# Performance work log

Measured on AMD Instinct MI355X. Metric: run time of the kernel, lower is better.

Reference implementation:

```python
import jax, jax.numpy as jnp
import numpy as np
import math

B, S, D, H = 2, 2048, 1024, 16
DH = D // H  # dim_per_head = 64


def setup_inputs() -> dict:
    key = jax.random.key(0)
    ks = jax.random.split(key, 12)
    s = 1.0 / math.sqrt(D)
    return {
        "key": jax.random.normal(ks[0], (B, S, D), jnp.float32),
        "value": jax.random.normal(ks[1], (B, S, D), jnp.float32),
        "query": jax.random.normal(ks[2], (B, S, D), jnp.float32),
        "mask": jax.random.randint(ks[3], (B, S, S), 0, 2).astype(bool),
        "Wq": jax.random.normal(ks[4], (D, D), jnp.float32) * s,
        "bq": jnp.zeros((D,), jnp.float32),
        "Wk": jax.random.normal(ks[5], (D, D), jnp.float32) * s,
        "bk": jnp.zeros((D,), jnp.float32),
        "Wv": jax.random.normal(ks[6], (D, D), jnp.float32) * s,
        "bv": jnp.zeros((D,), jnp.float32),
        "Wo": jax.random.normal(ks[7], (D, D), jnp.float32) * s,
        "bo": jnp.zeros((D,), jnp.float32),
    }


def _shape(x):
    # [B, S, D] -> [B, H, S, DH]
    return x.reshape(B, -1, H, DH).transpose(0, 2, 1, 3)


def reference(key, value, query, mask, Wq, bq, Wk, bk, Wv, bv, Wo, bo):
    q = _shape(query @ Wq.T + bq)  # [B,H,Sq,DH]
    k = _shape(key @ Wk.T + bk)    # [B,H,Sk,DH]
    v = _shape(value @ Wv.T + bv)  # [B,H,Sk,DH]
    q = q / jnp.sqrt(jnp.asarray(DH, q.dtype))
    scores = jnp.einsum("bhqd,bhkd->bhqk", q, k)
    scores = jnp.where(mask[:, None, :, :], jnp.asarray(-1e18, scores.dtype), scores)
    attn = jax.nn.softmax(scores, axis=-1)
    # dropout is identity in eval/deterministic reference
    ctx = jnp.einsum("bhqk,bhkd->bhqd", attn, v)
    ctx = ctx.transpose(0, 2, 1, 3).reshape(B, -1, D)  # unshape
    return ctx @ Wo.T + bo
```

## Files before the change

kernel.cpp:

```cpp
#include <hip/hip_runtime.h>
#include <math.h>


constexpr int Bc  = 2;
constexpr int Sc  = 2048;
constexpr int Dc  = 1024;
constexpr int Hc  = 16;
constexpr int DHc = 64;
constexpr int BSc = Bc * Sc;

constexpr float LOG2E = 1.4426950408889634f;

typedef __bf16 bf16x8 __attribute__((ext_vector_type(8)));
typedef __bf16 bf16x4 __attribute__((ext_vector_type(4)));
typedef float  f32x4  __attribute__((ext_vector_type(4)));

#define GLDS16(gp, lp) __builtin_amdgcn_global_load_lds( \
    (const __attribute__((address_space(1))) void*)(gp), \
    (__attribute__((address_space(3))) void*)(lp), 16, 0, 0)

__global__ __launch_bounds__(256)
void wsplit(const float* __restrict__ W0, const float* __restrict__ W1,
            const float* __restrict__ W2, const float* __restrict__ W3,
            __bf16* __restrict__ out)
{
    const float* src[4] = {W0, W1, W2, W3};
    const int z = blockIdx.y;
    const size_t idx = ((size_t)blockIdx.x * 256 + threadIdx.x) * 4;
    const float4 v = *(const float4*)&src[z][idx];
    bf16x4 o;
    o[0] = (__bf16)v.x; o[1] = (__bf16)v.y; o[2] = (__bf16)v.z; o[3] = (__bf16)v.w;
    *(bf16x4*)&out[(size_t)z * Dc * Dc + idx] = o;
}

__device__ __forceinline__ void sweep128s(const float* __restrict__ A,
                                          const __bf16* __restrict__ Wh,
                                          __bf16* As, __bf16* Ws,
                                          int gm0, int gn0, f32x4 acc[4][4])
{
    const int tid  = threadIdx.x;
    const int w    = tid >> 6;
    const int lane = tid & 63;
    const int cc   = lane & 15;
    const int g    = lane >> 4;
    const int wm   = (w & 1) * 64;
    const int wn   = (w >> 1) * 64;

    for (int k0 = 0; k0 < Dc; k0 += 64) {
        __syncthreads();
#pragma unroll
        for (int r = 0; r < 4; ++r) {
            const int L  = r * 256 + tid;
            const int wr = L >> 3;
            const int sl = L & 7;
            const int c  = sl ^ (wr & 7);
            GLDS16(Wh + (size_t)(gn0 + wr) * Dc + k0 + c * 8,
                   (char*)Ws + (r * 256 + w * 64) * 16);
        }
#pragma unroll
        for (int i = 0; i < 8; ++i) {
            const int Lq = i * 256 + tid;
            const int ar = Lq >> 4;
            const int aq = Lq & 15;
            const float4 v = *(const float4*)&A[(size_t)(gm0 + ar) * Dc + k0 + aq * 4];
            const int off = ar * 128 +
                        ((((aq >> 1) ^ (ar & 7)) << 4) | ((aq & 1) << 3));
            bf16x4 hv;
            hv[0] = (__bf16)v.x; hv[1] = (__bf16)v.y;
            hv[2] = (__bf16)v.z; hv[3] = (__bf16)v.w;
            *(bf16x4*)((char*)As + off) = hv;
        }
        __syncthreads();
#pragma unroll
        for (int kk = 0; kk < 2; ++kk) {
            const int cb4 = (kk * 4 + g) << 4;
            bf16x8 af[4], bfr[4];
#pragma unroll
            for (int mt = 0; mt < 4; ++mt) {
                const int row = wm + mt * 16 + cc;
                af[mt] = *(const bf16x8*)((const char*)As + row * 128 +
                                          (cb4 ^ ((row & 7) << 4)));
            }
#pragma unroll
            for (int nt = 0; nt < 4; ++nt) {
                const int row = wn + nt * 16 + cc;
                bfr[nt] = *(const bf16x8*)((const char*)Ws + row * 128 +
                                           (cb4 ^ ((row & 7) << 4)));
            }
#pragma unroll
            for (int mt = 0; mt < 4; ++mt)
#pragma unroll
                for (int nt = 0; nt < 4; ++nt)
                    acc[mt][nt] = __builtin_amdgcn_mfma_f32_16x16x32_bf16(
                        af[mt], bfr[nt], acc[mt][nt], 0, 0, 0);
        }
    }
}

__device__ __forceinline__ void sweep64b(const __bf16* __restrict__ Ahi,
                                         const __bf16* __restrict__ Alo,
                                         const __bf16* __restrict__ Wh,
                                         __bf16* AsHi, __bf16* AsLo, __bf16* Ws,
                                         int gm0, int gn0, f32x4 acc[2][4])
{
    const int tid  = threadIdx.x;
    const int w    = tid >> 6;
    const int lane = tid & 63;
    const int cc   = lane & 15;
    const int g    = lane >> 4;
    const int wm   = (w & 1) * 32;
    const int wn   = (w >> 1) * 64;

    for (int k0 = 0; k0 < Dc; k0 += 64) {
        __syncthreads();
#pragma unroll
        for (int r = 0; r < 4; ++r) {
            const int L  = r * 256 + tid;
            const int wr = L >> 3;
            const int sl = L & 7;
            const int c  = sl ^ (wr & 7);
            GLDS16(Wh + (size_t)(gn0 + wr) * Dc + k0 + c * 8,
                   (char*)Ws + (r * 256 + w * 64) * 16);
        }
#pragma unroll
        for (int r = 0; r < 2; ++r) {
            const int L  = r * 256 + tid;
            const int wr = L >> 3;
            const int sl = L & 7;
            const int c  = sl ^ (wr & 7);
            GLDS16(Ahi + (size_t)(gm0 + wr) * Dc + k0 + c * 8,
                   (char*)AsHi + (r * 256 + w * 64) * 16);
            GLDS16(Alo + (size_t)(gm0 + wr) * Dc + k0 + c * 8,
                   (char*)AsLo + (r * 256 + w * 64) * 16);
        }
        __syncthreads();
#pragma unroll
        for (int kk = 0; kk < 2; ++kk) {
            const int cb4 = (kk * 4 + g) << 4;
            bf16x8 ahi[2], alo[2], bfr[4];
#pragma unroll
            for (int mt = 0; mt < 2; ++mt) {
                const int row = wm + mt * 16 + cc;
                const int off = row * 128 + (cb4 ^ ((row & 7) << 4));
                ahi[mt] = *(const bf16x8*)((const char*)AsHi + off);
                alo[mt] = *(const bf16x8*)((const char*)AsLo + off);
            }
#pragma unroll
            for (int nt = 0; nt < 4; ++nt) {
                const int row = wn + nt * 16 + cc;
                bfr[nt] = *(const bf16x8*)((const char*)Ws + row * 128 +
                                           (cb4 ^ ((row & 7) << 4)));
            }
#pragma unroll
            for (int mt = 0; mt < 2; ++mt)
#pragma unroll
                for (int nt = 0; nt < 4; ++nt) {
                    acc[mt][nt] = __builtin_amdgcn_mfma_f32_16x16x32_bf16(
                        ahi[mt], bfr[nt], acc[mt][nt], 0, 0, 0);
                    acc[mt][nt] = __builtin_amdgcn_mfma_f32_16x16x32_bf16(
                        alo[mt], bfr[nt], acc[mt][nt], 0, 0, 0);
                }
        }
    }
}

__global__ __launch_bounds__(256)
void qkv_mfma(const float* __restrict__ query, const float* __restrict__ key,
              const float* __restrict__ value, const __bf16* __restrict__ Whi,
              const float* __restrict__ bq, const float* __restrict__ bk,
              const float* __restrict__ bv,
              __bf16* __restrict__ Qo, __bf16* __restrict__ Ko, __bf16* __restrict__ Vt)
{
    __shared__ __align__(16) __bf16 As[8192];
    __shared__ __align__(16) __bf16 Ws[8192];

    const int z = blockIdx.z;
    const float* A    = (z == 0) ? query : (z == 1) ? key : value;
    const float* bias = (z == 0) ? bq    : (z == 1) ? bk  : bv;
    const float scale = (z == 0) ? 0.125f * LOG2E : 1.0f;
    const __bf16* Wh  = Whi + (size_t)z * Dc * Dc;

    const int gm0 = blockIdx.x * 128;
    const int gn0 = blockIdx.y * 128;

    f32x4 acc[4][4];
#pragma unroll
    for (int mt = 0; mt < 4; ++mt)
#pragma unroll
        for (int nt = 0; nt < 4; ++nt) acc[mt][nt] = {0.f, 0.f, 0.f, 0.f};

    sweep128s(A, Wh, As, Ws, gm0, gn0, acc);

    const int tid = threadIdx.x;
    const int w = tid >> 6, lane = tid & 63;
    const int cc = lane & 15, g = lane >> 4;
    const int wm = (w & 1) * 64, wn = (w >> 1) * 64;

    float bias4[4];
#pragma unroll
    for (int nt = 0; nt < 4; ++nt) bias4[nt] = bias[gn0 + wn + nt * 16 + cc];

    if (z == 2) {
#pragma unroll
        for (int mt = 0; mt < 4; ++mt)
#pragma unroll
            for (int nt = 0; nt < 4; ++nt) {
                const int col = gn0 + wn + nt * 16 + cc;
                const int h = col >> 6, dh = col & 63;
                const int row0 = gm0 + wm + mt * 16 + g * 4;
                const int b = row0 >> 11, s0 = row0 & 2047;
                bf16x4 vv;
#pragma unroll
                for (int reg = 0; reg < 4; ++reg)
                    vv[reg] = (__bf16)(acc[mt][nt][reg] + bias4[nt]);
                *(bf16x4*)&Vt[(((size_t)(b * Hc + h)) * DHc + dh) * Sc + s0] = vv;
            }
    } else {
        __bf16* O = (z == 0) ? Qo : Ko;
#pragma unroll
        for (int mt = 0; mt < 4; ++mt)
#pragma unroll
            for (int nt = 0; nt < 4; ++nt) {
                const int col = gn0 + wn + nt * 16 + cc;
                const int h = col >> 6, dh = col & 63;
#pragma unroll
                for (int reg = 0; reg < 4; ++reg) {
                    const int row = gm0 + wm + mt * 16 + g * 4 + reg;
                    const int b = row >> 11, s = row & 2047;
                    O[(((size_t)(b * Hc + h)) * Sc + s) * DHc + dh] =
                        (__bf16)((acc[mt][nt][reg] + bias4[nt]) * scale);
                }
            }
    }
}

__global__ __launch_bounds__(256)
void out_mfma(const __bf16* __restrict__ ctxHi, const __bf16* __restrict__ ctxLo,
              const __bf16* __restrict__ Wohi,
              const float* __restrict__ bo, float* __restrict__ out)
{
    __shared__ __align__(16) __bf16 AsHi[4096];
    __shared__ __align__(16) __bf16 AsLo[4096];
    __shared__ __align__(16) __bf16 Ws[8192];

    const int gm0 = blockIdx.x * 64;
    const int gn0 = blockIdx.y * 128;

    f32x4 acc[2][4];
#pragma unroll
    for (int mt = 0; mt < 2; ++mt)
#pragma unroll
        for (int nt = 0; nt < 4; ++nt) acc[mt][nt] = {0.f, 0.f, 0.f, 0.f};

    sweep64b(ctxHi, ctxLo, Wohi, AsHi, AsLo, Ws, gm0, gn0, acc);

    const int tid = threadIdx.x;
    const int w = tid >> 6, lane = tid & 63;
    const int cc = lane & 15, g = lane >> 4;
    const int wm = (w & 1) * 32, wn = (w >> 1) * 64;

    float bias4[4];
#pragma unroll
    for (int nt = 0; nt < 4; ++nt) bias4[nt] = bo[gn0 + wn + nt * 16 + cc];

#pragma unroll
    for (int mt = 0; mt < 2; ++mt)
#pragma unroll
        for (int nt = 0; nt < 4; ++nt) {
            const int col = gn0 + wn + nt * 16 + cc;
#pragma unroll
            for (int reg = 0; reg < 4; ++reg) {
                const int row = gm0 + wm + mt * 16 + g * 4 + reg;
                out[(size_t)row * Dc + col] = acc[mt][nt][reg] + bias4[nt];
            }
        }
}

__global__ __launch_bounds__(256)
void mask_pack(const int* __restrict__ mask, unsigned long long* __restrict__ out)
{
    const int lane = threadIdx.x & 63;
    const size_t waveBase = ((size_t)blockIdx.x * 4 + (threadIdx.x >> 6)) * 256;
    unsigned long long b0 = __ballot(mask[waveBase + lane]        != 0);
    unsigned long long b1 = __ballot(mask[waveBase + 64 + lane]   != 0);
    unsigned long long b2 = __ballot(mask[waveBase + 128 + lane]  != 0);
    unsigned long long b3 = __ballot(mask[waveBase + 192 + lane]  != 0);
    if (lane == 0) {
        unsigned long long* dst = out + (waveBase >> 6);
        dst[0] = b0; dst[1] = b1; dst[2] = b2; dst[3] = b3;
    }
}

__global__ __launch_bounds__(256, 2)
void attn_mfma(const __bf16* __restrict__ Q, const __bf16* __restrict__ K,
               const __bf16* __restrict__ Vt,
               const unsigned long long* __restrict__ mp,
               __bf16* __restrict__ ctxHi, __bf16* __restrict__ ctxLo)
{
    __shared__ __align__(16) char smem[40960];

    const int tid  = threadIdx.x;
    const int w    = tid >> 6;
    const int lane = tid & 63;
    const int cc   = lane & 15;
    const int g    = lane >> 4;
    const int bh   = blockIdx.y;
    const int b    = bh >> 4;
    const int h    = bh & 15;
    const int qw   = blockIdx.x * 128 + w * 32;

    const __bf16* Qb  = Q  + (size_t)bh * Sc * DHc;
    const __bf16* Kb  = K  + (size_t)bh * Sc * DHc;
    const __bf16* Vtb = Vt + (size_t)bh * DHc * Sc;

    char* Pw = smem + 32768 + w * 2048;

    bf16x8 qa[2][2];
#pragma unroll
    for (int mt = 0; mt < 2; ++mt) {
        qa[mt][0] = *(const bf16x8*)&Qb[(size_t)(qw + mt * 16 + cc) * DHc + g * 8];
        qa[mt][1] = *(const bf16x8*)&Qb[(size_t)(qw + mt * 16 + cc) * DHc + 32 + g * 8];
    }

    f32x4 o[2][4] = {};
    float l[2][4] = {};

    const int ci[2] = {tid, 256 + tid};
    int  rowi[2], ski[2];
#pragma unroll
    for (int i = 0; i < 2; ++i) {
        rowi[i] = ci[i] >> 3;
        const int sl = ci[i] & 7;
        ski[i] = sl ^ (rowi[i] & 7);
    }

#pragma unroll
    for (int i = 0; i < 2; ++i) {
        GLDS16(Kb + (size_t)rowi[i] * DHc + ski[i] * 8,
               smem + ci[i] * 16);
        GLDS16(Vtb + (size_t)rowi[i] * Sc + ski[i] * 8,
               smem + 8192 + ci[i] * 16);
    }

    for (int it = 0; it < 32; ++it) {
        const int k0 = it * 64;
        char* Ks = smem + (it & 1) * 16384;
        char* Vs = Ks + 8192;

        __syncthreads();

        if (it + 1 < 32) {
            char* Kn = smem + ((it + 1) & 1) * 16384;
            const int kn = k0 + 64;
#pragma unroll
            for (int i = 0; i < 2; ++i) {
                GLDS16(Kb + (size_t)(kn + rowi[i]) * DHc + ski[i] * 8,
                       Kn + ci[i] * 16);
                GLDS16(Vtb + (size_t)rowi[i] * Sc + kn + ski[i] * 8,
                       Kn + 8192 + ci[i] * 16);
            }
        }

        unsigned long long mw[2][4];
#pragma unroll
        for (int mt = 0; mt < 2; ++mt)
#pragma unroll
            for (int r = 0; r < 4; ++r)
                mw[mt][r] = mp[(size_t)(b * Sc + qw + mt * 16 + g * 4 + r) * (Sc / 64)
                               + (k0 >> 6)];

        f32x4 sc[2][4];
#pragma unroll
        for (int nt = 0; nt < 4; ++nt) {
            const int row = nt * 16 + cc;
            const int rx  = (row & 7) << 4;
            const bf16x8 kb0 = *(const bf16x8*)(Ks + row * 128 + ((g << 4) ^ rx));
            const bf16x8 kb1 = *(const bf16x8*)(Ks + row * 128 + ((64 + (g << 4)) ^ rx));
            f32x4 z0 = {-24.f, -24.f, -24.f, -24.f};
            z0 = __builtin_amdgcn_mfma_f32_16x16x32_bf16(qa[0][0], kb0, z0, 0, 0, 0);
            z0 = __builtin_amdgcn_mfma_f32_16x16x32_bf16(qa[0][1], kb1, z0, 0, 0, 0);
            sc[0][nt] = z0;
            f32x4 z1 = {-24.f, -24.f, -24.f, -24.f};
            z1 = __builtin_amdgcn_mfma_f32_16x16x32_bf16(qa[1][0], kb0, z1, 0, 0, 0);
            z1 = __builtin_amdgcn_mfma_f32_16x16x32_bf16(qa[1][1], kb1, z1, 0, 0, 0);
            sc[1][nt] = z1;
        }

        bf16x8 pa[2][2];
#pragma unroll
        for (int mt = 0; mt < 2; ++mt) {
            unsigned mlo[4], mhi[4];
#pragma unroll
            for (int r = 0; r < 4; ++r) {
                const unsigned long long sh = mw[mt][r] >> cc;
                mlo[r] = (unsigned)sh;
                mhi[r] = (unsigned)(sh >> 32);
            }
#pragma unroll
            for (int nt = 0; nt < 4; ++nt)
#pragma unroll
                for (int r = 0; r < 4; ++r) {
                    float p = __builtin_amdgcn_exp2f(sc[mt][nt][r]);
                    const unsigned bit =
                        (nt == 0) ? (mlo[r] & 1u) :
                        (nt == 1) ? (mlo[r] & 0x10000u) :
                        (nt == 2) ? (mhi[r] & 1u) : (mhi[r] & 0x10000u);
                    p = bit ? 0.f : p;
                    l[mt][r] += p;
                    *(__bf16*)(Pw + (g * 4 + r) * 128 +
                               (((nt ^ g) << 5) | (cc << 1))) = (__bf16)p;
                }
            const int sw = (cc >> 2) << 5;
            pa[mt][0] = *(const bf16x8*)(Pw + cc * 128 + ((g * 16) ^ sw));
            pa[mt][1] = *(const bf16x8*)(Pw + cc * 128 + ((64 + g * 16) ^ sw));
        }

#pragma unroll
        for (int nt = 0; nt < 4; ++nt) {
            const int row = nt * 16 + cc;
            const int rx  = (row & 7) << 4;
            const bf16x8 vb0 = *(const bf16x8*)(Vs + row * 128 + ((g << 4) ^ rx));
            const bf16x8 vb1 = *(const bf16x8*)(Vs + row * 128 + ((64 + (g << 4)) ^ rx));
            o[0][nt] = __builtin_amdgcn_mfma_f32_16x16x32_bf16(pa[0][0], vb0, o[0][nt], 0, 0, 0);
            o[0][nt] = __builtin_amdgcn_mfma_f32_16x16x32_bf16(pa[0][1], vb1, o[0][nt], 0, 0, 0);
            o[1][nt] = __builtin_amdgcn_mfma_f32_16x16x32_bf16(pa[1][0], vb0, o[1][nt], 0, 0, 0);
            o[1][nt] = __builtin_amdgcn_mfma_f32_16x16x32_bf16(pa[1][1], vb1, o[1][nt], 0, 0, 0);
        }
    }

#pragma unroll
    for (int off = 1; off < 16; off <<= 1)
#pragma unroll
        for (int mt = 0; mt < 2; ++mt)
#pragma unroll
            for (int r = 0; r < 4; ++r)
                l[mt][r] += __shfl_xor(l[mt][r], off, 16);

#pragma unroll
    for (int mt = 0; mt < 2; ++mt)
#pragma unroll
        for (int r = 0; r < 4; ++r) {
            const float inv = 1.0f / l[mt][r];
            const int q = qw + mt * 16 + g * 4 + r;
#pragma unroll
            for (int nt = 0; nt < 4; ++nt) {
                const size_t idx = ((size_t)b * Sc + q) * Dc + h * 64 + nt * 16 + cc;
                const float v = o[mt][nt][r] * inv;
                const __bf16 hi = (__bf16)v;
                ctxHi[idx] = hi;
                ctxLo[idx] = (__bf16)(v - (float)hi);
            }
        }
}

extern "C" void kernel_launch(void* const* d_in, const int* in_sizes, int n_in,
                              void* d_out, int out_size, void* d_ws, size_t ws_size,
                              hipStream_t stream)
{
    const float* key   = (const float*)d_in[0];
    const float* value = (const float*)d_in[1];
    const float* query = (const float*)d_in[2];
    const int*   mask  = (const int*)  d_in[3];
    const float* Wq    = (const float*)d_in[4];
    const float* bq    = (const float*)d_in[5];
    const float* Wk    = (const float*)d_in[6];
    const float* bk    = (const float*)d_in[7];
    const float* Wv    = (const float*)d_in[8];
    const float* bv    = (const float*)d_in[9];
    const float* Wo    = (const float*)d_in[10];
    const float* bo    = (const float*)d_in[11];
    float* out = (float*)d_out;

    char* wsb = (char*)d_ws;
    __bf16* Qbf  = (__bf16*)(wsb);
    __bf16* Kbf  = (__bf16*)(wsb + ((size_t)8  << 20));
    __bf16* Vt   = (__bf16*)(wsb + ((size_t)16 << 20));
    unsigned long long* mpk = (unsigned long long*)(wsb + ((size_t)32 << 20));
    __bf16* Whi  = (__bf16*)(wsb + ((size_t)33 << 20));
    __bf16* ctxHi = (__bf16*)(wsb + ((size_t)41 << 20));
    __bf16* ctxLo = (__bf16*)(wsb + ((size_t)49 << 20));

    dim3 gws(Dc * Dc / (256 * 4), 4);
    wsplit<<<gws, 256, 0, stream>>>(Wq, Wk, Wv, Wo, Whi);

    dim3 gqkv(BSc / 128, Dc / 128, 3);
    qkv_mfma<<<gqkv, 256, 0, stream>>>(query, key, value, Whi, bq, bk, bv,
                                       Qbf, Kbf, Vt);

    const int mask_n = Bc * Sc * Sc;
    mask_pack<<<mask_n / 1024, 256, 0, stream>>>(mask, mpk);

    dim3 gattn(Sc / 128, Bc * Hc);
    attn_mfma<<<gattn, 256, 0, stream>>>(Qbf, Kbf, Vt, mpk, ctxHi, ctxLo);

    dim3 gout(BSc / 64, Dc / 128);
    out_mfma<<<gout, 256, 0, stream>>>(ctxHi, ctxLo, Whi + (size_t)3 * Dc * Dc,
                                       bo, out);
}
```

Measured before the change: 287.6 us.

## Double-buffer LDS tiles in QKV and output projection GEMM k-loops

Both projection GEMM sweeps now use two LDS buffers. The next k-tile is issued (async global-to-LDS copies for weights and bf16 activations, plus register prefetch of fp32 activations for QKV) before computing on the current tile, which cuts the loop to one barrier per iteration. This aims to hide global memory latency behind MFMA work. The cost is that LDS per block grows to 64KB and more registers are held for the prefetched activations, which may reduce occupancy.

```diff
diff --git a/kernel.cpp b/kernel.cpp
--- a/kernel.cpp
+++ b/kernel.cpp
@@ -33,9 +33,9 @@
     *(bf16x4*)&out[(size_t)z * Dc * Dc + idx] = o;
 }
 
-__device__ __forceinline__ void sweep128s(const float* __restrict__ A,
+__device__ __forceinline__ void sweep128p(const float* __restrict__ A,
                                           const __bf16* __restrict__ Wh,
-                                          __bf16* As, __bf16* Ws,
+                                          char* AsB, char* WsB,
                                           int gm0, int gn0, f32x4 acc[4][4])
 {
     const int tid  = threadIdx.x;
@@ -46,31 +46,56 @@
     const int wm   = (w & 1) * 64;
     const int wn   = (w >> 1) * 64;
 
-    for (int k0 = 0; k0 < Dc; k0 += 64) {
+    int wrow[4], wchk[4];
+#pragma unroll
+    for (int r = 0; r < 4; ++r) {
+        const int L = r * 256 + tid;
+        wrow[r] = L >> 3;
+        wchk[r] = (L & 7) ^ (wrow[r] & 7);
+    }
+
+    float4 av[8];
+#pragma unroll
+    for (int r = 0; r < 4; ++r)
+        GLDS16(Wh + (size_t)(gn0 + wrow[r]) * Dc + wchk[r] * 8,
+               WsB + (r * 256 + tid) * 16);
+#pragma unroll
+    for (int i = 0; i < 8; ++i) {
+        const int Lq = i * 256 + tid;
+        av[i] = *(const float4*)&A[(size_t)(gm0 + (Lq >> 4)) * Dc + (Lq & 15) * 4];
+    }
+#pragma unroll
+    for (int i = 0; i < 8; ++i) {
+        const int Lq = i * 256 + tid;
+        const int ar = Lq >> 4, aq = Lq & 15;
+        const int off = ar * 128 + ((((aq >> 1) ^ (ar & 7)) << 4) | ((aq & 1) << 3));
+        bf16x4 hv;
+        hv[0] = (__bf16)av[i].x; hv[1] = (__bf16)av[i].y;
+        hv[2] = (__bf16)av[i].z; hv[3] = (__bf16)av[i].w;
+        *(bf16x4*)(AsB + off) = hv;
+    }
+
+    for (int it = 0; it < Dc / 64; ++it) {
+        const char* As = AsB + (it & 1) * 16384;
+        const char* Ws = WsB + (it & 1) * 16384;
         __syncthreads();
-#pragma unroll
-        for (int r = 0; r < 4; ++r) {
-            const int L  = r * 256 + tid;
-            const int wr = L >> 3;
-            const int sl = L & 7;
-            const int c  = sl ^ (wr & 7);
-            GLDS16(Wh + (size_t)(gn0 + wr) * Dc + k0 + c * 8,
-                   (char*)Ws + (r * 256 + w * 64) * 16);
-        }
-#pragma unroll
-        for (int i = 0; i < 8; ++i) {
-            const int Lq = i * 256 + tid;
-            const int ar = Lq >> 4;
-            const int aq = Lq & 15;
-            const float4 v = *(const float4*)&A[(size_t)(gm0 + ar) * Dc + k0 + aq * 4];
-            const int off = ar * 128 +
-                        ((((aq >> 1) ^ (ar & 7)) << 4) | ((aq & 1) << 3));
-            bf16x4 hv;
-            hv[0] = (__bf16)v.x; hv[1] = (__bf16)v.y;
-            hv[2] = (__bf16)v.z; hv[3] = (__bf16)v.w;
-            *(bf16x4*)((char*)As + off) = hv;
-        }
-        __syncthreads();
+
+        const bool more = (it + 1 < Dc / 64);
+        if (more) {
+            const int kn = (it + 1) * 64;
+            char* Wn = WsB + ((it + 1) & 1) * 16384;
+#pragma unroll
+            for (int r = 0; r < 4; ++r)
+                GLDS16(Wh + (size_t)(gn0 + wrow[r]) * Dc + kn + wchk[r] * 8,
+                       Wn + (r * 256 + tid) * 16);
+#pragma unroll
+            for (int i = 0; i < 8; ++i) {
+                const int Lq = i * 256 + tid;
+                av[i] = *(const float4*)
+                    &A[(size_t)(gm0 + (Lq >> 4)) * Dc + kn + (Lq & 15) * 4];
+            }
+        }
+
 #pragma unroll
         for (int kk = 0; kk < 2; ++kk) {
             const int cb4 = (kk * 4 + g) << 4;
@@ -78,14 +103,12 @@
 #pragma unroll
             for (int mt = 0; mt < 4; ++mt) {
                 const int row = wm + mt * 16 + cc;
-                af[mt] = *(const bf16x8*)((const char*)As + row * 128 +
-                                          (cb4 ^ ((row & 7) << 4)));
+                af[mt] = *(const bf16x8*)(As + row * 128 + (cb4 ^ ((row & 7) << 4)));
             }
 #pragma unroll
             for (int nt = 0; nt < 4; ++nt) {
                 const int row = wn + nt * 16 + cc;
-                bfr[nt] = *(const bf16x8*)((const char*)Ws + row * 128 +
-                                           (cb4 ^ ((row & 7) << 4)));
+                bfr[nt] = *(const bf16x8*)(Ws + row * 128 + (cb4 ^ ((row & 7) << 4)));
             }
 #pragma unroll
             for (int mt = 0; mt < 4; ++mt)
@@ -94,13 +117,28 @@
                     acc[mt][nt] = __builtin_amdgcn_mfma_f32_16x16x32_bf16(
                         af[mt], bfr[nt], acc[mt][nt], 0, 0, 0);
         }
-    }
-}
-
-__device__ __forceinline__ void sweep64b(const __bf16* __restrict__ Ahi,
+
+        if (more) {
+            char* An = AsB + ((it + 1) & 1) * 16384;
+#pragma unroll
+            for (int i = 0; i < 8; ++i) {
+                const int Lq = i * 256 + tid;
+                const int ar = Lq >> 4, aq = Lq & 15;
+                const int off = ar * 128 +
+                                ((((aq >> 1) ^ (ar & 7)) << 4) | ((aq & 1) << 3));
+                bf16x4 hv;
+                hv[0] = (__bf16)av[i].x; hv[1] = (__bf16)av[i].y;
+                hv[2] = (__bf16)av[i].z; hv[3] = (__bf16)av[i].w;
+                *(bf16x4*)(An + off) = hv;
+            }
+        }
+    }
+}
+
+__device__ __forceinline__ void sweep64p(const __bf16* __restrict__ Ahi,
                                          const __bf16* __restrict__ Alo,
                                          const __bf16* __restrict__ Wh,
-                                         __bf16* AsHi, __bf16* AsLo, __bf16* Ws,
+                                         char* WsB, char* AhB, char* AlB,
                                          int gm0, int gn0, f32x4 acc[2][4])
 {
     const int tid  = threadIdx.x;
@@ -111,29 +149,57 @@
     const int wm   = (w & 1) * 32;
     const int wn   = (w >> 1) * 64;
 
-    for (int k0 = 0; k0 < Dc; k0 += 64) {
+    int wrow[4], wchk[4];
+#pragma unroll
+    for (int r = 0; r < 4; ++r) {
+        const int L = r * 256 + tid;
+        wrow[r] = L >> 3;
+        wchk[r] = (L & 7) ^ (wrow[r] & 7);
+    }
+    int arow[2], achk[2];
+#pragma unroll
+    for (int r = 0; r < 2; ++r) {
+        const int L = r * 256 + tid;
+        arow[r] = L >> 3;
+        achk[r] = (L & 7) ^ (arow[r] & 7);
+    }
+
+#pragma unroll
+    for (int r = 0; r < 4; ++r)
+        GLDS16(Wh + (size_t)(gn0 + wrow[r]) * Dc + wchk[r] * 8,
+               WsB + (r * 256 + tid) * 16);
+#pragma unroll
+    for (int r = 0; r < 2; ++r) {
+        GLDS16(Ahi + (size_t)(gm0 + arow[r]) * Dc + achk[r] * 8,
+               AhB + (r * 256 + tid) * 16);
+        GLDS16(Alo + (size_t)(gm0 + arow[r]) * Dc + achk[r] * 8,
+               AlB + (r * 256 + tid) * 16);
+    }
+
+    for (int it = 0; it < Dc / 64; ++it) {
+        const char* Ws = WsB + (it & 1) * 16384;
+        const char* Ah = AhB + (it & 1) * 8192;
+        const char* Al = AlB + (it & 1) * 8192;
         __syncthreads();
-#pragma unroll
-        for (int r = 0; r < 4; ++r) {
-            const int L  = r * 256 + tid;
-            const int wr = L >> 3;
-            const int sl = L & 7;
-            const int c  = sl ^ (wr & 7);
-            GLDS16(Wh + (size_t)(gn0 + wr) * Dc + k0 + c * 8,
-                   (char*)Ws + (r * 256 + w * 64) * 16);
-        }
-#pragma unroll
-        for (int r = 0; r < 2; ++r) {
-            const int L  = r * 256 + tid;
-            const int wr = L >> 3;
-            const int sl = L & 7;
-            const int c  = sl ^ (wr & 7);
-            GLDS16(Ahi + (size_t)(gm0 + wr) * Dc + k0 + c * 8,
-                   (char*)AsHi + (r * 256 + w * 64) * 16);
-            GLDS16(Alo + (size_t)(gm0 + wr) * Dc + k0 + c * 8,
-                   (char*)AsLo + (r * 256 + w * 64) * 16);
-        }
-        __syncthreads();
+
+        if (it + 1 < Dc / 64) {
+            const int kn = (it + 1) * 64;
+            char* Wn = WsB + ((it + 1) & 1) * 16384;
+            char* Hn = AhB + ((it + 1) & 1) * 8192;
+            char* Ln = AlB + ((it + 1) & 1) * 8192;
+#pragma unroll
+            for (int r = 0; r < 4; ++r)
+                GLDS16(Wh + (size_t)(gn0 + wrow[r]) * Dc + kn + wchk[r] * 8,
+                       Wn + (r * 256 + tid) * 16);
+#pragma unroll
+            for (int r = 0; r < 2; ++r) {
+                GLDS16(Ahi + (size_t)(gm0 + arow[r]) * Dc + kn + achk[r] * 8,
+                       Hn + (r * 256 + tid) * 16);
+                GLDS16(Alo + (size_t)(gm0 + arow[r]) * Dc + kn + achk[r] * 8,
+                       Ln + (r * 256 + tid) * 16);
+            }
+        }
+
 #pragma unroll
         for (int kk = 0; kk < 2; ++kk) {
             const int cb4 = (kk * 4 + g) << 4;
@@ -142,14 +208,13 @@
             for (int mt = 0; mt < 2; ++mt) {
                 const int row = wm + mt * 16 + cc;
                 const int off = row * 128 + (cb4 ^ ((row & 7) << 4));
-                ahi[mt] = *(const bf16x8*)((const char*)AsHi + off);
-                alo[mt] = *(const bf16x8*)((const char*)AsLo + off);
+                ahi[mt] = *(const bf16x8*)(Ah + off);
+                alo[mt] = *(const bf16x8*)(Al + off);
             }
 #pragma unroll
             for (int nt = 0; nt < 4; ++nt) {
                 const int row = wn + nt * 16 + cc;
-                bfr[nt] = *(const bf16x8*)((const char*)Ws + row * 128 +
-                                           (cb4 ^ ((row & 7) << 4)));
+                bfr[nt] = *(const bf16x8*)(Ws + row * 128 + (cb4 ^ ((row & 7) << 4)));
             }
 #pragma unroll
             for (int mt = 0; mt < 2; ++mt)
@@ -171,8 +236,7 @@
               const float* __restrict__ bv,
               __bf16* __restrict__ Qo, __bf16* __restrict__ Ko, __bf16* __restrict__ Vt)
 {
-    __shared__ __align__(16) __bf16 As[8192];
-    __shared__ __align__(16) __bf16 Ws[8192];
+    __shared__ __align__(16) char smem[65536];
 
     const int z = blockIdx.z;
     const float* A    = (z == 0) ? query : (z == 1) ? key : value;
@@ -189,7 +253,7 @@
 #pragma unroll
         for (int nt = 0; nt < 4; ++nt) acc[mt][nt] = {0.f, 0.f, 0.f, 0.f};
 
-    sweep128s(A, Wh, As, Ws, gm0, gn0, acc);
+    sweep128p(A, Wh, smem, smem + 32768, gm0, gn0, acc);
 
     const int tid = threadIdx.x;
     const int w = tid >> 6, lane = tid & 63;
@@ -239,9 +303,7 @@
               const __bf16* __restrict__ Wohi,
               const float* __restrict__ bo, float* __restrict__ out)
 {
-    __shared__ __align__(16) __bf16 AsHi[4096];
-    __shared__ __align__(16) __bf16 AsLo[4096];
-    __shared__ __align__(16) __bf16 Ws[8192];
+    __shared__ __align__(16) char smem[65536];
 
     const int gm0 = blockIdx.x * 64;
     const int gn0 = blockIdx.y * 128;
@@ -252,7 +314,7 @@
 #pragma unroll
         for (int nt = 0; nt < 4; ++nt) acc[mt][nt] = {0.f, 0.f, 0.f, 0.f};
 
-    sweep64b(ctxHi, ctxLo, Wohi, AsHi, AsLo, Ws, gm0, gn0, acc);
+    sweep64p(ctxHi, ctxLo, Wohi, smem, smem + 32768, smem + 49152, gm0, gn0, acc);
 
     const int tid = threadIdx.x;
     const int w = tid >> 6, lane = tid & 63;
```

Measured after the change: 273.2 us. 5.0% less time.
